# Performance work log

Measured on AMD Instinct MI355X. Metric: run time of the kernel, lower is better.

The kernel has to match this reference:

```python
import jax, jax.numpy as jnp
import numpy as np
from jax import lax

B, C, HW = 8, 512, 32
NH = 8            # num_heads
NG = 32           # num_groups
HD = C // NH      # head_size = 64
EPS = 1e-6


def group_norm(x, gamma, beta, groups=NG, eps=EPS):
    b, c, h, w = x.shape
    xr = x.reshape(b, groups, c // groups, h, w)
    mu = xr.mean(axis=(2, 3, 4), keepdims=True)
    var = xr.var(axis=(2, 3, 4), keepdims=True)
    xn = ((xr - mu) / jnp.sqrt(var + eps)).reshape(b, c, h, w)
    return xn * gamma[None, :, None, None] + beta[None, :, None, None]


def conv2d(x, w, b):
    y = lax.conv_general_dilated(x, w, (1, 1), 'SAME',
                                 dimension_numbers=('NCHW', 'OIHW', 'NCHW'))
    return y + b[None, :, None, None]


def setup_inputs() -> dict:
    key = jax.random.key(0)
    ks = jax.random.split(key, 24)
    f32 = jnp.float32

    def lin(k, out_d, in_d):
        return (jax.random.normal(k, (out_d, in_d), f32) / np.sqrt(in_d)).astype(f32)

    inp = {
        'hidden_states': jax.random.normal(ks[0], (B, C, HW, HW), f32),
        'pre_g': jnp.ones(C, f32), 'pre_b': jnp.zeros(C, f32),
        'norm_g': jnp.ones(C, f32), 'norm_b': jnp.zeros(C, f32),
        'post_g': jnp.ones(C, f32), 'post_b': jnp.zeros(C, f32),
        'pos_emb': jax.random.normal(ks[1], (1, C, 32, 32), f32) * 0.02,
        'sa_w1': (jax.random.normal(ks[2], (C // 8, C, 1, 1), f32) / np.sqrt(C)),
        'sa_b1': jnp.zeros(C // 8, f32),
        'sa_w2': (jax.random.normal(ks[3], (C // 8, C // 8, 3, 3), f32) / np.sqrt(9 * C // 8)),
        'sa_b2': jnp.zeros(C // 8, f32),
        'sa_w3': (jax.random.normal(ks[4], (1, C // 8, 1, 1), f32) / np.sqrt(C // 8)),
        'sa_b3': jnp.zeros(1, f32),
        'wq': lin(ks[5], C, C), 'wk': lin(ks[6], C, C), 'wv': lin(ks[7], C, C),
        'wq0': lin(ks[8], C // 2, C), 'wk0': lin(ks[9], C // 2, C), 'wv0': lin(ks[10], C // 2, C),
        'wq1': lin(ks[11], C // 2, C), 'wk1': lin(ks[12], C // 2, C), 'wv1': lin(ks[13], C // 2, C),
        'ff_w1': lin(ks[14], C, 2 * C), 'ff_b1': jnp.zeros(C, f32),
        'ff_w2': lin(ks[15], C, C), 'ff_b2': jnp.zeros(C, f32),
        'out_w': lin(ks[16], C, C), 'out_b': jnp.zeros(C, f32),
    }
    return inp


def reference(hidden_states, pre_g, pre_b, norm_g, norm_b, post_g, post_b,
              pos_emb, sa_w1, sa_b1, sa_w2, sa_b2, sa_w3, sa_b3,
              wq, wk, wv, wq0, wk0, wv0, wq1, wk1, wv1,
              ff_w1, ff_b1, ff_w2, ff_b2, out_w, out_b):
    b, c, h, w = hidden_states.shape
    S = h * w
    residual = hidden_states

    hs = group_norm(hidden_states, pre_g, pre_b)
    # H=W=32 matches pos_embedding; bilinear resize to same size is identity
    hs = hs + pos_emb

    # spatial attention gating (conv 1x1 -> SiLU -> conv 3x3 -> SiLU -> conv 1x1 -> sigmoid)
    a = jax.nn.silu(conv2d(hs, sa_w1, sa_b1))
    a = jax.nn.silu(conv2d(a, sa_w2, sa_b2))
    spatial_weights = jax.nn.sigmoid(conv2d(a, sa_w3, sa_b3))
    spatial_enhanced = hs * spatial_weights

    # standard multi-head self-attention over flattened tokens
    sh = group_norm(hs, norm_g, norm_b).reshape(b, c, S).transpose(0, 2, 1)  # (B,S,C)
    ehs = sh  # encoder_hidden_states defaults to standard_hidden

    q = (sh @ wq.T).reshape(b, S, NH, HD)
    k = (ehs @ wk.T).reshape(b, S, NH, HD)
    v = (ehs @ wv.T).reshape(b, S, NH, HD)
    scores = jnp.einsum('bqhd,bkhd->bhqk', q, k) / np.sqrt(HD)
    probs = jax.nn.softmax(scores, axis=-1)
    std_out = jnp.einsum('bhqk,bkhd->bqhd', probs, v).reshape(b, S, c)

    # two multi-scale single-head attention branches (dim C/2 each)
    msh = spatial_enhanced.reshape(b, c, S).transpose(0, 2, 1)  # (B,S,C)
    parts = []
    for wqm, wkm, wvm in ((wq0, wk0, wv0), (wq1, wk1, wv1)):
        qm = msh @ wqm.T          # (B,S,C/2)
        km = ehs @ wkm.T
        vm = ehs @ wvm.T
        sc = jnp.einsum('bqd,bkd->bqk', qm, km) / np.sqrt(c // 2)
        parts.append(jnp.einsum('bqk,bkd->bqd', jax.nn.softmax(sc, axis=-1), vm))
    multi_out = jnp.concatenate(parts, axis=-1)  # (B,S,C)

    combined = jnp.concatenate([std_out, multi_out], axis=-1)  # (B,S,2C)
    fused = jax.nn.silu(combined @ ff_w1.T + ff_b1) @ ff_w2.T + ff_b2  # dropout = eval identity
    final = fused @ out_w.T + out_b
    final = final.transpose(0, 2, 1).reshape(b, c, h, w)
    final = group_norm(final, post_g, post_b)
    return final + residual
```

## Files before the change

### kernel.cpp

```cpp
#include <hip/hip_runtime.h>
#include <hip/hip_bf16.h>
#include <math.h>

typedef __attribute__((ext_vector_type(8))) __bf16 v8bf;
typedef __attribute__((ext_vector_type(4))) float v4f;

__device__ __forceinline__ unsigned short f2bf(float f) {
  union { float f; unsigned int u; } a; a.f = f;
  unsigned int r = a.u + 0x7fffu + ((a.u >> 16) & 1u);
  return (unsigned short)(r >> 16);
}
__device__ __forceinline__ unsigned short f2bf_trunc(float f) {
  union { float f; unsigned int u; } a; a.f = f;
  return (unsigned short)(a.u >> 16);
}
__device__ __forceinline__ float bf2f(unsigned short u) {
  union { unsigned int i; float f; } a; a.i = ((unsigned int)u) << 16; return a.f;
}
__device__ __forceinline__ float sigm(float x) { return 1.0f / (1.0f + __expf(-x)); }

__device__ __forceinline__ void async16(const void* g, void* l) {
  __builtin_amdgcn_global_load_lds(
      (const __attribute__((address_space(1))) unsigned int*)g,
      (__attribute__((address_space(3))) unsigned int*)l, 16, 0, 0);
}

__global__ __launch_bounds__(256) void gn_pre_kernel(
    const float* __restrict__ x, const float* __restrict__ g, const float* __restrict__ be,
    const float* __restrict__ pos, unsigned short* __restrict__ hsb, float* __restrict__ stats) {
  __shared__ float L[16384];
  __shared__ float rs[4], rs2[4], mr[2];
  int b = blockIdx.x >> 5, grp = blockIdx.x & 31;
  const float4* base = (const float4*)(x + ((size_t)b*512 + grp*16)*1024);
  float4* L4 = (float4*)L;
  int w = threadIdx.x >> 6;
  float s = 0.f, s2 = 0.f;
  for (int i = threadIdx.x; i < 4096; i += 256) {
    float4 v = base[i];
    L4[i] = v;
    s += v.x + v.y + v.z + v.w;
    s2 += v.x*v.x + v.y*v.y + v.z*v.z + v.w*v.w;
  }
#pragma unroll
  for (int o = 32; o; o >>= 1) { s += __shfl_xor(s, o); s2 += __shfl_xor(s2, o); }
  if ((threadIdx.x & 63) == 0) { rs[w] = s; rs2[w] = s2; }
  __syncthreads();
  if (threadIdx.x == 0) {
    float ts = rs[0]+rs[1]+rs[2]+rs[3], ts2 = rs2[0]+rs2[1]+rs2[2]+rs2[3];
    float mu = ts * (1.0f/16384.0f);
    float var = ts2 * (1.0f/16384.0f) - mu*mu;
    mr[0] = mu; mr[1] = rsqrtf(var + 1e-6f);
  }
  __syncthreads();
  float mu = mr[0], rstd = mr[1];
  const float4* pb = (const float4*)(pos + (size_t)grp*16*1024);
  float ns = 0.f, ns2 = 0.f;
  for (int i = threadIdx.x; i < 4096; i += 256) {
    float4 v = L4[i], p = pb[i];
    int c = grp*16 + (i >> 8);
    float gg = g[c], bb = be[c];
    float4 o;
    o.x = (v.x - mu)*rstd*gg + bb + p.x;
    o.y = (v.y - mu)*rstd*gg + bb + p.y;
    o.z = (v.z - mu)*rstd*gg + bb + p.z;
    o.w = (v.w - mu)*rstd*gg + bb + p.w;
    L4[i] = o;
    ns += o.x + o.y + o.z + o.w;
    ns2 += o.x*o.x + o.y*o.y + o.z*o.z + o.w*o.w;
  }
#pragma unroll
  for (int o = 32; o; o >>= 1) { ns += __shfl_xor(ns, o); ns2 += __shfl_xor(ns2, o); }
  if ((threadIdx.x & 63) == 0) { rs[w] = ns; rs2[w] = ns2; }
  __syncthreads();
  if (threadIdx.x == 0) {
    float ts = rs[0]+rs[1]+rs[2]+rs[3], ts2 = rs2[0]+rs2[1]+rs2[2]+rs2[3];
    float nmu = ts * (1.0f/16384.0f);
    float nvar = ts2 * (1.0f/16384.0f) - nmu*nmu;
    stats[(b*32+grp)*2] = nmu; stats[(b*32+grp)*2+1] = rsqrtf(nvar + 1e-6f);
  }
#pragma unroll
  for (int j = 0; j < 4; ++j) {
    int sI = threadIdx.x + j*256;
    unsigned int wd[8];
#pragma unroll
    for (int c = 0; c < 8; ++c) {
      unsigned int lo = f2bf(L[(2*c)*1024 + sI]);
      unsigned int hi = f2bf(L[(2*c+1)*1024 + sI]);
      wd[c] = lo | (hi << 16);
    }
    size_t oo = (size_t)(b*1024 + sI)*512 + grp*16;
    *(uint4*)(hsb + oo)     = make_uint4(wd[0], wd[1], wd[2], wd[3]);
    *(uint4*)(hsb + oo + 8) = make_uint4(wd[4], wd[5], wd[6], wd[7]);
  }
}

__global__ __launch_bounds__(256) void im2col_kernel(
    const unsigned short* __restrict__ a1, unsigned short* __restrict__ im2) {
  int row0 = blockIdx.x * 8;
#pragma unroll
  for (int it = 0; it < 3; ++it) {
    int cc = it*256 + threadIdx.x;
    if (cc >= 576) break;
    int rl = cc / 72, rr = cc - rl*72;
    int tap = rr >> 3, ch8 = rr & 7;
    int row = row0 + rl;
    int bb = row >> 10, s = row & 1023;
    int y = s >> 5, xx0 = s & 31;
    int yy = y + tap/3 - 1, xx = xx0 + tap%3 - 1;
    ushort4 v0 = make_ushort4(0,0,0,0), v1 = make_ushort4(0,0,0,0);
    if ((unsigned)yy < 32u && (unsigned)xx < 32u) {
      const unsigned short* src = a1 + ((size_t)(bb*1024 + yy*32 + xx))*64 + ch8*8;
      v0 = *(const ushort4*)src; v1 = *(const ushort4*)(src + 4);
    }
    unsigned short* dst = im2 + (size_t)row*576 + tap*64 + ch8*8;
    *(ushort4*)dst = v0; *(ushort4*)(dst + 4) = v1;
  }
}

__global__ __launch_bounds__(256) void gate_norm_kernel(
    const unsigned short* __restrict__ hsb, const unsigned short* __restrict__ a2,
    const float* __restrict__ w3, const float* __restrict__ b3,
    const float* __restrict__ stats, const float* __restrict__ g,
    const float* __restrict__ be,
    unsigned short* __restrict__ sh, unsigned short* __restrict__ msh) {
  int b = blockIdx.y;
  int s = blockIdx.x * 4 + (threadIdx.x >> 6);
  int oct = threadIdx.x & 63;
  int c0 = oct * 8;
  int grp = c0 >> 4;
  float part = bf2f(a2[((size_t)(b*1024) + s)*64 + oct]) * w3[oct];
#pragma unroll
  for (int o = 32; o; o >>= 1) part += __shfl_xor(part, o);
  float wgt = sigm(part + b3[0]);
  float mu = stats[(b*32 + grp)*2], rstd = stats[(b*32 + grp)*2 + 1];
  size_t o = (size_t)(b*1024 + s)*512 + c0;
  ushort4 u0 = *(const ushort4*)(hsb + o), u1 = *(const ushort4*)(hsb + o + 4);
  unsigned short uu[8] = {u0.x,u0.y,u0.z,u0.w,u1.x,u1.y,u1.z,u1.w};
  unsigned short so[8], mo[8];
#pragma unroll
  for (int j = 0; j < 8; ++j) {
    float v = bf2f(uu[j]);
    so[j] = f2bf((v - mu)*rstd*g[c0+j] + be[c0+j]);
    mo[j] = f2bf(v * wgt);
  }
  *(ushort4*)(sh + o)     = make_ushort4(so[0], so[1], so[2], so[3]);
  *(ushort4*)(sh + o + 4) = make_ushort4(so[4], so[5], so[6], so[7]);
  *(ushort4*)(msh + o)     = make_ushort4(mo[0], mo[1], mo[2], mo[3]);
  *(ushort4*)(msh + o + 4) = make_ushort4(mo[4], mo[5], mo[6], mo[7]);
}

struct WCvt { const float* src; int dstOff; int n; float scale; };
struct WCvtArgs { WCvt w[15]; };
__global__ __launch_bounds__(256) void wconvert_kernel(WCvtArgs a, unsigned short* __restrict__ dst) {
  WCvt e = a.w[blockIdx.y];
  int i = blockIdx.x * 256 + threadIdx.x;
  if (i >= e.n) return;
  if (blockIdx.y == 13) {
    int oc = i / 576, r = i - oc*576;
    int tap = r >> 6, ic = r & 63;
    dst[e.dstOff + i] = f2bf(e.src[(oc*64 + ic)*9 + tap]);
  } else if (blockIdx.y == 14) {
    dst[e.dstOff + i] = f2bf(e.src[(i & 511)*512 + (i >> 9)]);
  } else {
    dst[e.dstOff + i] = f2bf(e.src[i] * e.scale);
  }
}

__global__ __launch_bounds__(256) void bias_fold_kernel(
    const float* __restrict__ ow, const float* __restrict__ b2,
    const float* __restrict__ ob, float* __restrict__ bc) {
  int n = blockIdx.x * 256 + threadIdx.x;
  float s = ob[n];
  const float* r = ow + (size_t)n * 512;
#pragma unroll 8
  for (int j = 0; j < 512; ++j) s += r[j] * b2[j];
  bc[n] = s;
}

__global__ __launch_bounds__(256) void transpose2_kernel(
    const unsigned short* __restrict__ qkvm,
    unsigned short* __restrict__ vtb, unsigned short* __restrict__ vmt) {
  __shared__ unsigned short t[64][65];
  int s0 = blockIdx.x * 64, c0 = blockIdx.y * 64;
  int z = blockIdx.z, b = z & 7;
  const unsigned short* in = qkvm + (z >= 8 ? 2048 : 1024);
  unsigned short* out = (z >= 8) ? vmt : vtb;
  int tx = threadIdx.x & 63, ty = threadIdx.x >> 6;
#pragma unroll
  for (int i = 0; i < 16; ++i) {
    int s = ty + i*4;
    t[s][tx] = in[((size_t)(b*1024 + s0 + s))*2560 + c0 + tx];
  }
  __syncthreads();
#pragma unroll
  for (int i = 0; i < 16; ++i) {
    int c = ty + i*4;
    out[((size_t)b*512 + c0 + c)*1024 + s0 + tx] = t[tx][c];
  }
}

struct GemmDesc {
  const unsigned short* A; const unsigned short* B; void* out; const float* bias;
  int M, N, K, lda, ldb, ldo, epi;
  long long Ay, Az, By, Bz, Oy, Oz;
};

template<int BM, int BN>
__global__ __launch_bounds__(256) void gemm_tile_kernel(GemmDesc d) {
  constexpr int WGM = (BN >= 128) ? 2 : 4;
  constexpr int WGN = 4 / WGM;
  constexpr int MT = BM / (16 * WGM);
  constexpr int NT = BN / (16 * WGN);
  constexpr int AIT = (BM * 8) / 256;
  constexpr int BIT = (BN * 8) / 256;
  __shared__ __align__(16) unsigned short As[BM * 64];
  __shared__ __align__(16) unsigned short Bs[BN * 64];

  int ntx = d.N / BN, mtx = d.M / BM;
  int bmt, bnt;
  if ((mtx & 7) == 0) {
    int xcd = blockIdx.x & 7, j = blockIdx.x >> 3;
    int mpx = mtx >> 3;
    bmt = xcd * mpx + (j % mpx);
    bnt = j / mpx;
  } else {
    bmt = blockIdx.x / ntx; bnt = blockIdx.x % ntx;
  }
  int bm0 = bmt * BM, bn0 = bnt * BN;
  const unsigned short* A = d.A + (long long)blockIdx.y * d.Ay
      + (long long)blockIdx.z * d.Az + (size_t)bm0 * d.lda;
  const unsigned short* B = d.B + (long long)blockIdx.y * d.By
      + (long long)blockIdx.z * d.Bz + (size_t)bn0 * d.ldb;
  int tid = threadIdx.x, lane = tid & 63, w = tid >> 6;
  int wm = (WGN == 2) ? (w >> 1) : w;
  int wn = (WGN == 2) ? (w & 1) : 0;
  int ln = lane & 15, qd = lane >> 4;

  v4f acc[MT][NT];
#pragma unroll
  for (int i = 0; i < MT; ++i)
#pragma unroll
    for (int j = 0; j < NT; ++j) acc[i][j] = (v4f){0.f, 0.f, 0.f, 0.f};

  int nks = d.K >> 6;
  for (int ks = 0; ks < nks; ++ks) {
    int kof = ks * 64;
#pragma unroll
    for (int it = 0; it < AIT; ++it) {
      int c = it * 256 + tid;
      int row = c >> 3, ch = c & 7;
      async16(A + (size_t)row * d.lda + ((ch ^ (row & 7)) << 3) + kof, As + c * 8);
    }
#pragma unroll
    for (int it = 0; it < BIT; ++it) {
      int c = it * 256 + tid;
      int row = c >> 3, ch = c & 7;
      async16(B + (size_t)row * d.ldb + ((ch ^ (row & 7)) << 3) + kof, Bs + c * 8);
    }
    __syncthreads();
#pragma unroll
    for (int k2 = 0; k2 < 2; ++k2) {
      v8bf af[MT], bfr[NT];
#pragma unroll
      for (int i = 0; i < MT; ++i) {
        int row = wm * MT * 16 + i * 16 + ln;
        af[i] = *(const v8bf*)(As + row * 64 + (((k2*4 + qd) ^ (ln & 7)) << 3));
      }
#pragma unroll
      for (int j = 0; j < NT; ++j) {
        int row = wn * NT * 16 + j * 16 + ln;
        bfr[j] = *(const v8bf*)(Bs + row * 64 + (((k2*4 + qd) ^ (ln & 7)) << 3));
      }
#pragma unroll
      for (int i = 0; i < MT; ++i)
#pragma unroll
        for (int j = 0; j < NT; ++j)
          acc[i][j] = __builtin_amdgcn_mfma_f32_16x16x32_bf16(af[i], bfr[j], acc[i][j], 0, 0, 0);
    }
    __syncthreads();
  }

  size_t obase = (size_t)((long long)blockIdx.y * d.Oy + (long long)blockIdx.z * d.Oz);
#pragma unroll
  for (int i = 0; i < MT; ++i) {
#pragma unroll
    for (int j = 0; j < NT; ++j) {
      int col = bn0 + wn * NT * 16 + j * 16 + ln;
      float bia = d.bias ? d.bias[col] : 0.0f;
#pragma unroll
      for (int r = 0; r < 4; ++r) {
        int row = bm0 + wm * MT * 16 + i * 16 + qd * 4 + r;
        float v = acc[i][j][r] + bia;
        if (d.epi == 2) v = v * sigm(v);
        size_t oi = obase + (size_t)row * d.ldo + col;
        if (d.epi == 0) ((float*)d.out)[oi] = v;
        else ((unsigned short*)d.out)[oi] = f2bf(v);
      }
    }
  }
}

__global__ __launch_bounds__(512) void flash_attn_kernel(
    const unsigned short* __restrict__ QKVM, const unsigned short* __restrict__ VTB,
    unsigned short* __restrict__ out) {
  __shared__ __align__(16) unsigned short Ks[128*64];
  __shared__ __align__(16) unsigned short Vts[64*128];
  __shared__ __align__(16) unsigned short Pw[8][16*128];
  int h = blockIdx.x, b = blockIdx.y, qt = blockIdx.z;
  int tid = threadIdx.x, lane = tid & 63, w = tid >> 6;
  int ln = lane & 15, qd = lane >> 4;

  const unsigned short* Qbase = QKVM + ((size_t)(b*1024 + qt*128 + w*16))*2560 + h*64;
  v8bf aq[2];
#pragma unroll
  for (int s = 0; s < 2; ++s)
    aq[s] = *(const v8bf*)(Qbase + (size_t)ln*2560 + s*32 + qd*8);

  v4f o_acc[4];
  float l_part[4];
#pragma unroll
  for (int dn = 0; dn < 4; ++dn) o_acc[dn] = (v4f){0.f,0.f,0.f,0.f};
#pragma unroll
  for (int r = 0; r < 4; ++r) l_part[r] = 0.f;

  const unsigned short* Kg = QKVM + 512 + (size_t)(b*1024)*2560 + h*64;
  const unsigned short* Vg = VTB + ((size_t)(b*512) + h*64)*1024;

  for (int kt = 0; kt < 8; ++kt) {
#pragma unroll
    for (int it = 0; it < 2; ++it) {
      int c = it*512 + tid;
      async16(Kg + (size_t)(kt*128 + (c >> 3))*2560 + (((c & 7) ^ ((c >> 3) & 7)) << 3),
              Ks + c*8);
    }
#pragma unroll
    for (int it = 0; it < 2; ++it) {
      int c = it*512 + tid;
      async16(Vg + (size_t)(c >> 4)*1024 + kt*128 + ((((c & 15) ^ ((c >> 4) & 7))) << 3),
              Vts + c*8);
    }
    __syncthreads();

    v4f sc[8];
#pragma unroll
    for (int n = 0; n < 8; ++n) {
      v4f a = (v4f){0.f,0.f,0.f,0.f};
#pragma unroll
      for (int s = 0; s < 2; ++s) {
        v8bf kb = *(const v8bf*)(Ks + (n*16 + ln)*64 + (((s*4 + qd) ^ (ln & 7)) << 3));
        a = __builtin_amdgcn_mfma_f32_16x16x32_bf16(aq[s], kb, a, 0, 0, 0);
      }
      sc[n] = a;
    }
#pragma unroll
    for (int r = 0; r < 4; ++r) {
      int row7 = (qd*4 + r) & 7;
      float acc_l = 0.f;
#pragma unroll
      for (int n = 0; n < 8; ++n) {
        float p = exp2f(sc[n][r]);
        acc_l += p;
        Pw[w][(qd*4 + r)*128 + (((n*2 + (ln >> 3)) ^ row7) << 3) + (ln & 7)] = f2bf_trunc(p);
      }
      l_part[r] += acc_l;
    }
#pragma unroll
    for (int dn = 0; dn < 4; ++dn) {
      v4f a = o_acc[dn];
#pragma unroll
      for (int ks2 = 0; ks2 < 4; ++ks2) {
        int phys = (((ks2*4 + qd) ^ (ln & 7)) << 3);
        v8bf pf = *(const v8bf*)(&Pw[w][ln*128 + phys]);
        v8bf vf = *(const v8bf*)(Vts + (dn*16 + ln)*128 + phys);
        a = __builtin_amdgcn_mfma_f32_16x16x32_bf16(pf, vf, a, 0, 0, 0);
      }
      o_acc[dn] = a;
    }
    __syncthreads();
  }

  unsigned short* ob = out + ((size_t)(b*1024 + qt*128 + w*16))*1024 + h*64;
#pragma unroll
  for (int r = 0; r < 4; ++r) {
    float l = l_part[r];
    l += __shfl_xor(l, 1); l += __shfl_xor(l, 2);
    l += __shfl_xor(l, 4); l += __shfl_xor(l, 8);
    float rinv = 1.0f / l;
#pragma unroll
    for (int dn = 0; dn < 4; ++dn)
      ob[(size_t)(qd*4 + r)*1024 + dn*16 + ln] = f2bf(o_acc[dn][r] * rinv);
  }
}

__global__ __launch_bounds__(256) void flash_branch_kernel(
    const unsigned short* __restrict__ QKVM, const unsigned short* __restrict__ QM,
    const unsigned short* __restrict__ VMT, unsigned short* __restrict__ out) {
  __shared__ __align__(16) unsigned short Ks[64*256];
  __shared__ __align__(16) unsigned short Vts[256*64];
  __shared__ __align__(16) unsigned short Pw[4][16*64];
  int bb = blockIdx.x, b = bb >> 1, br = bb & 1;
  int qt = blockIdx.z;
  int tid = threadIdx.x, lane = tid & 63, w = tid >> 6;
  int ln = lane & 15, qd = lane >> 4;

  const unsigned short* Qb = QM + ((size_t)(b*1024 + qt*64 + w*16))*512 + br*256;
  v8bf aq[8];
#pragma unroll
  for (int s = 0; s < 8; ++s)
    aq[s] = *(const v8bf*)(Qb + (size_t)ln*512 + s*32 + qd*8);

  v4f o_acc[16];
  float l_part[4];
#pragma unroll
  for (int dn = 0; dn < 16; ++dn) o_acc[dn] = (v4f){0.f,0.f,0.f,0.f};
#pragma unroll
  for (int r = 0; r < 4; ++r) l_part[r] = 0.f;

  const unsigned short* Kg = QKVM + 1536 + br*256 + (size_t)(b*1024)*2560;
  const unsigned short* Vg = VMT + ((size_t)(b*512) + br*256)*1024;

  for (int kt = 0; kt < 16; ++kt) {
#pragma unroll
    for (int it = 0; it < 8; ++it) {
      int c = it*256 + tid;
      int row = c >> 5, ch = c & 31;
      async16(Kg + (size_t)(kt*64 + row)*2560 + ((ch ^ (row & 7)) << 3), Ks + c*8);
    }
#pragma unroll
    for (int it = 0; it < 8; ++it) {
      int c = it*256 + tid;
      int row = c >> 3, ch = c & 7;
      async16(Vg + (size_t)row*1024 + kt*64 + ((ch ^ (row & 7)) << 3), Vts + c*8);
    }
    __syncthreads();

    v4f sc[4];
#pragma unroll
    for (int n = 0; n < 4; ++n) {
      v4f a = (v4f){0.f,0.f,0.f,0.f};
      int krow = n*16 + ln;
#pragma unroll
      for (int s = 0; s < 8; ++s) {
        v8bf kb = *(const v8bf*)(Ks + krow*256 + (((s*4 + qd) ^ (krow & 7)) << 3));
        a = __builtin_amdgcn_mfma_f32_16x16x32_bf16(aq[s], kb, a, 0, 0, 0);
      }
      sc[n] = a;
    }
#pragma unroll
    for (int r = 0; r < 4; ++r) {
      int row7 = (qd*4 + r) & 7;
      float acc_l = 0.f;
#pragma unroll
      for (int n = 0; n < 4; ++n) {
        float p = exp2f(sc[n][r]);
        acc_l += p;
        Pw[w][(qd*4 + r)*64 + (((n*2 + (ln >> 3)) ^ row7) << 3) + (ln & 7)] = f2bf_trunc(p);
      }
      l_part[r] += acc_l;
    }
#pragma unroll
    for (int dn = 0; dn < 16; ++dn) {
      v4f a = o_acc[dn];
#pragma unroll
      for (int ks2 = 0; ks2 < 2; ++ks2) {
        int phys = (((ks2*4 + qd) ^ (ln & 7)) << 3);
        v8bf pf = *(const v8bf*)(&Pw[w][ln*64 + phys]);
        v8bf vf = *(const v8bf*)(Vts + (dn*16 + ln)*64 + phys);
        a = __builtin_amdgcn_mfma_f32_16x16x32_bf16(pf, vf, a, 0, 0, 0);
      }
      o_acc[dn] = a;
    }
    __syncthreads();
  }

  unsigned short* ob = out + ((size_t)(b*1024 + qt*64 + w*16))*1024 + 512 + br*256;
#pragma unroll
  for (int r = 0; r < 4; ++r) {
    float l = l_part[r];
    l += __shfl_xor(l, 1); l += __shfl_xor(l, 2);
    l += __shfl_xor(l, 4); l += __shfl_xor(l, 8);
    float rinv = 1.0f / l;
#pragma unroll
    for (int dn = 0; dn < 16; ++dn)
      ob[(size_t)(qd*4 + r)*1024 + dn*16 + ln] = f2bf(o_acc[dn][r] * rinv);
  }
}

__global__ __launch_bounds__(256) void gn_stats_bf16_kernel(
    const unsigned short* __restrict__ t, float* __restrict__ stats) {
  int b = blockIdx.x >> 5, grp = blockIdx.x & 31;
  float s = 0.f, s2 = 0.f;
#pragma unroll
  for (int j = 0; j < 4; ++j) {
    int sI = threadIdx.x + j*256;
    const unsigned short* p = t + ((size_t)(b*1024 + sI))*512 + grp*16;
    uint4 a = *(const uint4*)p, c2 = *(const uint4*)(p + 8);
    unsigned int ww[8] = {a.x,a.y,a.z,a.w,c2.x,c2.y,c2.z,c2.w};
#pragma unroll
    for (int k = 0; k < 8; ++k) {
      float lo = bf2f((unsigned short)(ww[k] & 0xffff));
      float hi = bf2f((unsigned short)(ww[k] >> 16));
      s += lo + hi; s2 += lo*lo + hi*hi;
    }
  }
#pragma unroll
  for (int o = 32; o; o >>= 1) { s += __shfl_xor(s, o); s2 += __shfl_xor(s2, o); }
  __shared__ float rs[4], rs2[4];
  int w = threadIdx.x >> 6;
  if ((threadIdx.x & 63) == 0) { rs[w] = s; rs2[w] = s2; }
  __syncthreads();
  if (threadIdx.x == 0) {
    float ts = rs[0]+rs[1]+rs[2]+rs[3], ts2 = rs2[0]+rs2[1]+rs2[2]+rs2[3];
    float mu = ts * (1.0f/16384.0f);
    float var = ts2 * (1.0f/16384.0f) - mu*mu;
    stats[(b*32+grp)*2] = mu; stats[(b*32+grp)*2+1] = rsqrtf(var + 1e-6f);
  }
}

__global__ __launch_bounds__(256) void final_out_kernel(
    const unsigned short* __restrict__ fin, const float* __restrict__ stats,
    const float* __restrict__ g, const float* __restrict__ be,
    const float* __restrict__ x, float* __restrict__ out) {
  __shared__ float t[64][65];
  int s0 = blockIdx.x * 64, c0 = blockIdx.y * 64, b = blockIdx.z;
  int tx = threadIdx.x & 63, ty = threadIdx.x >> 6;
#pragma unroll
  for (int i = 0; i < 16; ++i) {
    int s = ty + i*4;
    t[s][tx] = bf2f(fin[((size_t)(b*1024 + s0 + s))*512 + c0 + tx]);
  }
  __syncthreads();
#pragma unroll
  for (int i = 0; i < 16; ++i) {
    int c = ty + i*4;
    int cc = c0 + c, grp = cc >> 4;
    float mu = stats[(b*32+grp)*2], rstd = stats[(b*32+grp)*2+1];
    float gg = g[cc], bb = be[cc];
    size_t oi = ((size_t)(b*512 + cc))*1024 + s0 + tx;
    out[oi] = (t[tx][c] - mu)*rstd*gg + bb + x[oi];
  }
}

static void launch_gemm128(hipStream_t st, const unsigned short* A, const unsigned short* B,
                           void* out, const float* bias,
                           int M, int N, int K, int lda, int ldb, int ldo, int epi,
                           long long Ay, long long Az, long long By, long long Bz,
                           long long Oy, long long Oz, int gy, int gz) {
  GemmDesc d{A, B, out, bias, M, N, K, lda, ldb, ldo, epi, Ay, Az, By, Bz, Oy, Oz};
  gemm_tile_kernel<128,128><<<dim3((M/128)*(N/128), gy, gz), dim3(256), 0, st>>>(d);
}
static void launch_gemm64(hipStream_t st, const unsigned short* A, const unsigned short* B,
                          void* out, const float* bias,
                          int M, int N, int K, int lda, int ldb, int ldo, int epi) {
  GemmDesc d{A, B, out, bias, M, N, K, lda, ldb, ldo, epi, 0,0,0,0,0,0};
  gemm_tile_kernel<128,64><<<dim3((M/128)*(N/64), 1, 1), dim3(256), 0, st>>>(d);
}

extern "C" void kernel_launch(void* const* d_in, const int* in_sizes, int n_in,
                              void* d_out, int out_size, void* d_ws, size_t ws_size,
                              hipStream_t stream) {
  const float* x      = (const float*)d_in[0];
  const float* pre_g  = (const float*)d_in[1];
  const float* pre_b  = (const float*)d_in[2];
  const float* norm_g = (const float*)d_in[3];
  const float* norm_b = (const float*)d_in[4];
  const float* post_g = (const float*)d_in[5];
  const float* post_b = (const float*)d_in[6];
  const float* pos    = (const float*)d_in[7];
  const float* sa_b1  = (const float*)d_in[9];
  const float* sa_b2  = (const float*)d_in[11];
  const float* sa_w3  = (const float*)d_in[12];
  const float* sa_b3  = (const float*)d_in[13];
  const float* ff_b1  = (const float*)d_in[24];
  const float* ff_b2  = (const float*)d_in[26];
  const float* out_w  = (const float*)d_in[27];
  const float* out_b  = (const float*)d_in[28];
  float* outp = (float*)d_out;

  char* ws = (char*)d_ws;
  size_t off = 0;
  auto alloc = [&](size_t bytes) -> void* {
    void* p = ws + off; off += (bytes + 255) & ~(size_t)255; return p;
  };
  float* STATS = (float*)alloc(4096);
  float* BC    = (float*)alloc(2048);
  unsigned short* HSB  = (unsigned short*)alloc(8388608);
  unsigned short* A1   = (unsigned short*)alloc(1048576);
  unsigned short* IM2  = (unsigned short*)alloc(9437184);
  unsigned short* A2   = (unsigned short*)alloc(1048576);
  unsigned short* SHB  = (unsigned short*)alloc(8388608);
  unsigned short* MSHB = (unsigned short*)alloc(8388608);
  unsigned short* WBF  = (unsigned short*)alloc(6291456);
  unsigned short* WCOMB= (unsigned short*)alloc(524288);
  unsigned short* QKVM = (unsigned short*)alloc(41943040);
  unsigned short* QM   = (unsigned short*)alloc(8388608);
  unsigned short* VTB  = (unsigned short*)alloc(8388608);
  unsigned short* VMT  = (unsigned short*)alloc(8388608);
  unsigned short* COMB = (unsigned short*)alloc(16777216);
  unsigned short* FFMID= (unsigned short*)alloc(8388608);
  unsigned short* FINALB=(unsigned short*)alloc(8388608);

  const int OQKVM=0, OQM=1310720, OFF1=1572864, OFF2T=2097152,
            OOW=2359296, OW1=2621440, OW2R=2654208;

  gn_pre_kernel<<<dim3(256), dim3(256), 0, stream>>>(x, pre_g, pre_b, pos, HSB, STATS);
  {
    WCvtArgs a;
    const float LG2E = 1.4426950408889634f;
    const int   srcIdx[15] = {14,15,16, 18,21,19,22, 17,20, 23,27, 8, 0, 10, 25};
    const int   dofs[15]   = {0, 262144, 524288,
                              786432, 917504, 1048576, 1179648,
                              OQM, OQM+131072,
                              OFF1, OOW, OW1, 0, OW2R, OFF2T};
    const int   ns[15]     = {262144,262144,262144, 131072,131072,131072,131072,
                              131072,131072, 524288,262144, 32768, 0, 36864, 262144};
    const float sc[15]     = {0.125f*LG2E,1.f,1.f, 1.f,1.f,1.f,1.f,
                              0.0625f*LG2E,0.0625f*LG2E, 1.f,1.f, 1.f, 0.f, 1.f, 1.f};
    for (int i = 0; i < 15; ++i) { a.w[i].src = (const float*)d_in[srcIdx[i]]; a.w[i].dstOff = dofs[i]; a.w[i].n = ns[i]; a.w[i].scale = sc[i]; }
    wconvert_kernel<<<dim3(2048, 15), dim3(256), 0, stream>>>(a, WBF);
  }
  {
    GemmDesc d{WBF+OOW, WBF+OFF2T, WCOMB, nullptr, 512, 512, 512, 512, 512, 512, 1, 0,0,0,0,0,0};
    gemm_tile_kernel<128,128><<<dim3(16, 1, 1), dim3(256), 0, stream>>>(d);
  }
  bias_fold_kernel<<<dim3(2), dim3(256), 0, stream>>>(out_w, ff_b2, out_b, BC);
  launch_gemm64(stream, HSB, WBF+OW1,  A1, sa_b1, 8192, 64, 512, 512, 512, 64, 2);
  im2col_kernel<<<dim3(1024), dim3(256), 0, stream>>>(A1, IM2);
  launch_gemm64(stream, IM2, WBF+OW2R, A2, sa_b2, 8192, 64, 576, 576, 576, 64, 2);
  gate_norm_kernel<<<dim3(256, 8), dim3(256), 0, stream>>>(HSB, A2, sa_w3, sa_b3, STATS, norm_g, norm_b, SHB, MSHB);

  launch_gemm128(stream, SHB,  WBF+OQKVM, QKVM, nullptr, 8192, 2560, 512, 512, 512, 2560, 1, 0,0,0,0,0,0, 1,1);
  launch_gemm64(stream, MSHB, WBF+OQM,   QM,   nullptr, 8192, 512,  512, 512, 512, 512,  1);

  transpose2_kernel<<<dim3(16, 8, 16), dim3(256), 0, stream>>>(QKVM, VTB, VMT);

  flash_attn_kernel<<<dim3(8, 8, 8), dim3(512), 0, stream>>>(QKVM, VTB, COMB);

  flash_branch_kernel<<<dim3(16, 1, 16), dim3(256), 0, stream>>>(QKVM, QM, VMT, COMB);

  launch_gemm64(stream, COMB,  WBF+OFF1, FFMID,  ff_b1, 8192, 512, 1024, 1024, 1024, 512, 2);
  launch_gemm64(stream, FFMID, WCOMB,    FINALB, BC,    8192, 512, 512,  512,  512,  512, 1);

  gn_stats_bf16_kernel<<<dim3(256), dim3(256), 0, stream>>>(FINALB, STATS);
  final_out_kernel<<<dim3(16, 8, 8), dim3(256), 0, stream>>>(FINALB, STATS, post_g, post_b, x, outp);

  (void)in_sizes; (void)n_in; (void)out_size; (void)ws_size;
}
```

Before: 384.7 us.

## Split branch attention over two key halves and combine partials in a separate kernel

Splits the multi-scale branch flash-attention kernel's key loop into two halves along a new grid dimension, doubling the number of blocks. Each half writes unnormalized fp32 output and row sums to a workspace. A new combine kernel adds the two halves, normalizes, and writes bf16 into the combined buffer. This targets low block-level parallelism in the branch kernel, at the cost of an extra launch and extra fp32 partial traffic through global memory.

```diff
diff --git a/kernel.cpp b/kernel.cpp
--- a/kernel.cpp
+++ b/kernel.cpp
@@ -394,12 +394,12 @@
 
 __global__ __launch_bounds__(256) void flash_branch_kernel(
     const unsigned short* __restrict__ QKVM, const unsigned short* __restrict__ QM,
-    const unsigned short* __restrict__ VMT, unsigned short* __restrict__ out) {
+    const unsigned short* __restrict__ VMT, float* __restrict__ OP, float* __restrict__ LP) {
   __shared__ __align__(16) unsigned short Ks[64*256];
   __shared__ __align__(16) unsigned short Vts[256*64];
   __shared__ __align__(16) unsigned short Pw[4][16*64];
   int bb = blockIdx.x, b = bb >> 1, br = bb & 1;
-  int qt = blockIdx.z;
+  int kh = blockIdx.y, qt = blockIdx.z;
   int tid = threadIdx.x, lane = tid & 63, w = tid >> 6;
   int ln = lane & 15, qd = lane >> 4;
 
@@ -419,7 +419,7 @@
   const unsigned short* Kg = QKVM + 1536 + br*256 + (size_t)(b*1024)*2560;
   const unsigned short* Vg = VMT + ((size_t)(b*512) + br*256)*1024;
 
-  for (int kt = 0; kt < 16; ++kt) {
+  for (int kt = kh*8; kt < kh*8 + 8; ++kt) {
 #pragma unroll
     for (int it = 0; it < 8; ++it) {
       int c = it*256 + tid;
@@ -473,16 +473,41 @@
     __syncthreads();
   }
 
-  unsigned short* ob = out + ((size_t)(b*1024 + qt*64 + w*16))*1024 + 512 + br*256;
+  int slot = ((bb*16 + qt)*2 + kh);
+  float* Ob = OP + (size_t)slot*16384;
+  float* Lb = LP + (size_t)slot*64;
 #pragma unroll
   for (int r = 0; r < 4; ++r) {
+    int row = w*16 + qd*4 + r;
     float l = l_part[r];
     l += __shfl_xor(l, 1); l += __shfl_xor(l, 2);
     l += __shfl_xor(l, 4); l += __shfl_xor(l, 8);
-    float rinv = 1.0f / l;
+    if (ln == 0) Lb[row] = l;
 #pragma unroll
     for (int dn = 0; dn < 16; ++dn)
-      ob[(size_t)(qd*4 + r)*1024 + dn*16 + ln] = f2bf(o_acc[dn][r] * rinv);
+      Ob[(size_t)row*256 + dn*16 + ln] = o_acc[dn][r];
+  }
+}
+
+__global__ __launch_bounds__(256) void branch_combine_kernel(
+    const float* __restrict__ OP, const float* __restrict__ LP,
+    unsigned short* __restrict__ out) {
+  int bb = blockIdx.x, qt = blockIdx.y;
+  int b = bb >> 1, br = bb & 1;
+  int slot0 = (bb*16 + qt)*2, slot1 = slot0 + 1;
+  int row = threadIdx.x >> 2, cseg = (threadIdx.x & 3) * 64;
+  float l = LP[(size_t)slot0*64 + row] + LP[(size_t)slot1*64 + row];
+  float rinv = 1.0f / l;
+  const float4* o0 = (const float4*)(OP + (size_t)slot0*16384 + (size_t)row*256 + cseg);
+  const float4* o1 = (const float4*)(OP + (size_t)slot1*16384 + (size_t)row*256 + cseg);
+  unsigned short* ob = out + ((size_t)(b*1024 + qt*64 + row))*1024 + 512 + br*256 + cseg;
+#pragma unroll
+  for (int i = 0; i < 16; ++i) {
+    float4 a = o0[i], c = o1[i];
+    ob[i*4+0] = f2bf((a.x + c.x) * rinv);
+    ob[i*4+1] = f2bf((a.y + c.y) * rinv);
+    ob[i*4+2] = f2bf((a.z + c.z) * rinv);
+    ob[i*4+3] = f2bf((a.w + c.w) * rinv);
   }
 }
 
@@ -599,6 +624,8 @@
   unsigned short* COMB = (unsigned short*)alloc(16777216);
   unsigned short* FFMID= (unsigned short*)alloc(8388608);
   unsigned short* FINALB=(unsigned short*)alloc(8388608);
+  float* OP    = (float*)alloc(33554432);
+  float* LP    = (float*)alloc(131072);
 
   const int OQKVM=0, OQM=1310720, OFF1=1572864, OFF2T=2097152,
             OOW=2359296, OW1=2621440, OW2R=2654208;
@@ -636,7 +663,8 @@
 
   flash_attn_kernel<<<dim3(8, 8, 8), dim3(512), 0, stream>>>(QKVM, VTB, COMB);
 
-  flash_branch_kernel<<<dim3(16, 1, 16), dim3(256), 0, stream>>>(QKVM, QM, VMT, COMB);
+  flash_branch_kernel<<<dim3(16, 2, 16), dim3(256), 0, stream>>>(QKVM, QM, VMT, OP, LP);
+  branch_combine_kernel<<<dim3(16, 16), dim3(256), 0, stream>>>(OP, LP, COMB);
 
   launch_gemm64(stream, COMB,  WBF+OFF1, FFMID,  ff_b1, 8192, 512, 1024, 1024, 1024, 512, 2);
   launch_gemm64(stream, FFMID, WCOMB,    FINALB, BC,    8192, 512, 512,  512,  512,  512, 1);
```

Result: slower. 402.0 us (+4.5%).
